# Kernel tuning notes

Hardware: AMD Instinct MI355X
Metric: run time of the kernel (lower is better)

The kernel has to match this reference:

```python
import jax, jax.numpy as jnp
import numpy as np

B, S, D, H, M = 4, 512, 768, 12, 4
DFF = 4 * D
HD = D // H
EPS = 1e-6  # timm/jvp_layers LayerNorm eps
SCALE = HD ** -0.5


def _ln(x, g, b):
    mu = jnp.mean(x, axis=-1, keepdims=True)
    var = jnp.mean((x - mu) ** 2, axis=-1, keepdims=True)
    return (x - mu) * jax.lax.rsqrt(var + EPS) * g + b


def _block(x, g1, b1, Wqkv, Wproj, bproj, g2, b2, W1, bf1, W2, bf2):
    # pre-norm attention
    h = _ln(x, g1, b1)
    qkv = h @ Wqkv                       # [B,S,3D]
    q, k, v = jnp.split(qkv, 3, axis=-1)
    q = q.reshape(B, S, H, HD)
    k = k.reshape(B, S, H, HD)
    v = v.reshape(B, S, H, HD)
    scores = jnp.einsum('bqhd,bkhd->bhqk', q, k) * SCALE
    attn = jax.nn.softmax(scores, axis=-1)
    o = jnp.einsum('bhqk,bkhd->bqhd', attn, v).reshape(B, S, D)
    x = x + o @ Wproj + bproj
    # pre-norm MLP
    h2 = _ln(x, g2, b2)
    mlp = jax.nn.gelu(h2 @ W1 + bf1, approximate=False) @ W2 + bf2
    return x + mlp


def setup_inputs() -> dict:
    key = jax.random.key(0)
    ks = jax.random.split(key, 8)
    w = 0.02
    return {
        'x': jax.random.normal(ks[0], (B, S, D), jnp.float32),
        'x_tangent': jax.random.normal(ks[1], (B, M, S, D), jnp.float32),
        'g1': jnp.ones((D,), jnp.float32),
        'b1': jnp.zeros((D,), jnp.float32),
        'Wqkv': jax.random.normal(ks[2], (D, 3 * D), jnp.float32) * w,
        'Wproj': jax.random.normal(ks[3], (D, D), jnp.float32) * w,
        'bproj': jnp.zeros((D,), jnp.float32),
        'g2': jnp.ones((D,), jnp.float32),
        'b2': jnp.zeros((D,), jnp.float32),
        'W1': jax.random.normal(ks[4], (D, DFF), jnp.float32) * w,
        'bf1': jnp.zeros((DFF,), jnp.float32),
        'W2': jax.random.normal(ks[5], (DFF, D), jnp.float32) * w,
        'bf2': jnp.zeros((D,), jnp.float32),
    }


def reference(x, x_tangent, g1, b1, Wqkv, Wproj, bproj, g2, b2, W1, bf1, W2, bf2):
    f = lambda xx: _block(xx, g1, b1, Wqkv, Wproj, bproj, g2, b2, W1, bf1, W2, bf2)
    # linearize once: primal + efficient JVP for all M tangent directions
    out, jvp_fn = jax.linearize(f, x)
    out_tangent = jax.vmap(jvp_fn, in_axes=1, out_axes=1)(x_tangent)  # [B,M,S,D]
    return out, out_tangent
```

## Files before the change

kernel.cpp:

```cpp
#include <hip/hip_runtime.h>
#include <math.h>

constexpr int B_ = 4, S_ = 512, D_ = 768, H_ = 12, M_ = 4, DFF_ = 3072, HD_ = 64;
constexpr float EPS_ = 1e-6f;
constexpr float SCALE_ = 0.125f;
constexpr int BS_ = B_ * S_;
constexpr int BH_ = B_ * H_;
constexpr long long BSD_ = (long long)BS_ * D_;
constexpr long long BS3D_ = (long long)BS_ * 3 * D_;
constexpr long long ATT_ = (long long)BH_ * S_ * S_;
constexpr long long BSF_ = (long long)BS_ * DFF_;

typedef __attribute__((ext_vector_type(8))) short bf16x8;
typedef __attribute__((ext_vector_type(4))) float f32x4;

__device__ __forceinline__ ushort f2bf(float f) {
    uint32_t u = __float_as_uint(f);
    u += 0x7FFF + ((u >> 16) & 1);
    return (ushort)(u >> 16);
}
__device__ __forceinline__ float bf2f(ushort u) {
    return __uint_as_float((uint32_t)u << 16);
}

__device__ __forceinline__ void gll16(const ushort* g, ushort* l) {
    __builtin_amdgcn_global_load_lds((const __attribute__((address_space(1))) void*)g,
                                     (__attribute__((address_space(3))) void*)l, 16, 0, 0);
}

template <int N> __device__ __forceinline__ void waitcnt_vm() {
    if constexpr (N == 0) asm volatile("s_waitcnt vmcnt(0)" ::: "memory");
    else if constexpr (N == 4) asm volatile("s_waitcnt vmcnt(4)" ::: "memory");
    else if constexpr (N == 6) asm volatile("s_waitcnt vmcnt(6)" ::: "memory");
    else if constexpr (N == 8) asm volatile("s_waitcnt vmcnt(8)" ::: "memory");
    else static_assert(N == 0 || N == 4 || N == 6 || N == 8, "add literal");
}

__device__ __forceinline__ void waitcnt_lgkm0() {
    asm volatile("s_waitcnt lgkmcnt(0)" ::: "memory");
    __builtin_amdgcn_sched_barrier(0);
}

__device__ __forceinline__ int xcd_swz(int flat, int nwg) {
    int q = nwg >> 3, r = nwg & 7;
    int x = flat & 7, pos = flat >> 3;
    int base = (x < r) ? x * (q + 1) : r * (q + 1) + (x - r) * q;
    return base + pos;
}

__device__ __forceinline__ size_t stroff(int rg, int c, int Nc) {
    int m = rg >> 11;
    int b = (rg >> 9) & (B_ - 1);
    int s = rg & (S_ - 1);
    return ((size_t)((b * M_ + m) * S_ + s)) * Nc + c;
}

__device__ __forceinline__ float block_sum(float v) {
    __shared__ float red[4];
    int tid = threadIdx.x;
#pragma unroll
    for (int off = 32; off > 0; off >>= 1) v += __shfl_down(v, off, 64);
    __syncthreads();
    if ((tid & 63) == 0) red[tid >> 6] = v;
    __syncthreads();
    return red[0] + red[1] + red[2] + red[3];
}

__device__ __forceinline__ float block_max(float v) {
    __shared__ float red[4];
    int tid = threadIdx.x;
#pragma unroll
    for (int off = 32; off > 0; off >>= 1) v = fmaxf(v, __shfl_down(v, off, 64));
    __syncthreads();
    if ((tid & 63) == 0) red[tid >> 6] = v;
    __syncthreads();
    return fmaxf(fmaxf(red[0], red[1]), fmaxf(red[2], red[3]));
}

__global__ __launch_bounds__(256) void transpose_f2b(const float* __restrict__ W,
                                                     ushort* __restrict__ WT,
                                                     int K, int N) {
    __shared__ float t[32][33];
    int n0 = blockIdx.x * 32, k0 = blockIdx.y * 32;
    int tx = threadIdx.x & 31, ty = threadIdx.x >> 5;
#pragma unroll
    for (int i = 0; i < 4; i++)
        t[ty + i * 8][tx] = W[(size_t)(k0 + ty + i * 8) * N + n0 + tx];
    __syncthreads();
#pragma unroll
    for (int i = 0; i < 4; i++)
        WT[(size_t)(n0 + ty + i * 8) * K + k0 + tx] = f2bf(t[tx][ty + i * 8]);
}

__global__ __launch_bounds__(256) void transpose_v(const ushort* __restrict__ src0,
                                                   ushort* __restrict__ Vt0,
                                                   ushort* __restrict__ dVt4) {
    int z = blockIdx.z;
    int m = z / BH_, bh = z % BH_;
    const ushort* qkvb = src0 + (size_t)m * BS3D_;
    ushort* Vt = (m == 0) ? Vt0 : dVt4 + (size_t)(m - 1) * BSD_;
    int b = bh / H_, hh = bh - b * H_;
    int s0 = blockIdx.x * 32, d0 = blockIdx.y * 32;
    __shared__ ushort t[32][33];
    int tx = threadIdx.x & 31, ty = threadIdx.x >> 5;
#pragma unroll
    for (int i = 0; i < 4; i++)
        t[ty + i * 8][tx] = qkvb[(size_t)(b * S_ + s0 + ty + i * 8) * 3 * D_ + 2 * D_ + hh * HD_ + d0 + tx];
    __syncthreads();
#pragma unroll
    for (int i = 0; i < 4; i++)
        Vt[(size_t)bh * HD_ * S_ + (size_t)(d0 + ty + i * 8) * S_ + s0 + tx] = t[tx][ty + i * 8];
}

__global__ __launch_bounds__(256) void ln_fwd(const float* __restrict__ x,
                                              const float* __restrict__ g,
                                              const float* __restrict__ bta,
                                              ushort* __restrict__ xhat,
                                              ushort* __restrict__ h,
                                              float* __restrict__ rstd) {
    int row = blockIdx.x;
    const float* xr = x + (size_t)row * D_;
    int tid = threadIdx.x;
    float v[3];
    float s = 0.f;
#pragma unroll
    for (int i = 0; i < 3; i++) { v[i] = xr[tid + i * 256]; s += v[i]; }
    s = block_sum(s);
    float mu = s * (1.0f / D_);
    float vs = 0.f;
#pragma unroll
    for (int i = 0; i < 3; i++) { float c = v[i] - mu; vs += c * c; }
    vs = block_sum(vs);
    float rs = rsqrtf(vs * (1.0f / D_) + EPS_);
#pragma unroll
    for (int i = 0; i < 3; i++) {
        int c = tid + i * 256;
        float xh = (v[i] - mu) * rs;
        xhat[(size_t)row * D_ + c] = f2bf(xh);
        h[(size_t)row * D_ + c] = f2bf(xh * g[c] + bta[c]);
    }
    if (tid == 0) rstd[row] = rs;
}

__global__ __launch_bounds__(256) void ln_jvp(const float* __restrict__ tf,
                                              const ushort* __restrict__ tb, int mode,
                                              const ushort* __restrict__ xhat,
                                              const float* __restrict__ rstd,
                                              const float* __restrict__ g,
                                              ushort* __restrict__ dh,
                                              ushort* __restrict__ xtb) {
    int rg = blockIdx.x;
    int r = rg & (BS_ - 1);
    size_t pbase = (size_t)r * D_;
    int tid = threadIdx.x;
    float tv[3], xh[3];
    float s1 = 0.f, s2 = 0.f;
    size_t tbase;
    if (mode == 0) {
        int m = rg >> 11;
        int b = r >> 9, s = r & (S_ - 1);
        tbase = ((size_t)((b * M_ + m) * S_ + s)) * D_;
    } else {
        tbase = (size_t)rg * D_;
    }
#pragma unroll
    for (int i = 0; i < 3; i++) {
        int c = tid + i * 256;
        tv[i] = (mode == 0) ? tf[tbase + c] : bf2f(tb[tbase + c]);
        xh[i] = bf2f(xhat[pbase + c]);
        s1 += tv[i];
        s2 += tv[i] * xh[i];
    }
    s1 = block_sum(s1);
    s2 = block_sum(s2);
    float mt = s1 * (1.0f / D_);
    float mx = s2 * (1.0f / D_);
    float rs = rstd[r];
#pragma unroll
    for (int i = 0; i < 3; i++) {
        int c = tid + i * 256;
        dh[(size_t)rg * D_ + c] = f2bf(g[c] * rs * (tv[i] - mt - xh[i] * mx));
        if (mode == 0 && xtb) xtb[(size_t)rg * D_ + c] = f2bf(tv[i]);
    }
}

template <int BM, int BN, int EPI, bool RS, bool OS>
__global__ __launch_bounds__(256) void gemm_mfma(const ushort* __restrict__ A,
                                                 const ushort* __restrict__ BT,
                                                 const float* __restrict__ bias,
                                                 const float* __restrict__ resf,
                                                 const ushort* __restrict__ resb,
                                                 float* __restrict__ Cf,
                                                 ushort* __restrict__ Cb,
                                                 ushort* __restrict__ aux,
                                                 int Nc, int Kd) {
    constexpr int FI = BM / 32, FJ = BN / 32;
    constexpr int LA = BM / 32, LB = BN / 32, L = LA + LB;
    __shared__ ushort As[2][BM * 64];
    __shared__ ushort Bs[2][BN * 64];
    int tid = threadIdx.x;
    int wave = tid >> 6, lane = tid & 63;
    int wr = wave >> 1, wc = wave & 1;
    int gx = gridDim.x, nwg = gx * gridDim.y;
    int work = xcd_swz(blockIdx.x + blockIdx.y * gx, nwg);
    int band = work / (8 * gx);
    int wi = work - band * (8 * gx);
    int row0 = (band * 8 + (wi & 7)) * BM;
    int col0 = (wi >> 3) * BN;

    int srow = lane >> 3;
    int skel = ((lane & 7) ^ (lane >> 3)) * 8;
    const ushort* Ag0 = A + (size_t)(row0 + srow) * Kd + skel;
    const ushort* Bg0 = BT + (size_t)(col0 + srow) * Kd + skel;

    auto stage = [&](int bufi, int k0) {
#pragma unroll
        for (int cc = 0; cc < LA; cc++) {
            int c = wave * LA + cc;
            gll16(Ag0 + (size_t)(c * 8) * Kd + k0, As[bufi] + c * 512);
        }
#pragma unroll
        for (int cc = 0; cc < LB; cc++) {
            int c = wave * LB + cc;
            gll16(Bg0 + (size_t)(c * 8) * Kd + k0, Bs[bufi] + c * 512);
        }
    };

    int frow = lane & 15, fkb = (lane >> 4) * 8;
    int aoff[2][FI], boff[2][FJ];
#pragma unroll
    for (int ks = 0; ks < 2; ks++) {
        int sw = (fkb + ks * 32) ^ ((frow & 7) * 8);
#pragma unroll
        for (int i = 0; i < FI; i++) aoff[ks][i] = (wr * (BM / 2) + i * 16 + frow) * 64 + sw;
#pragma unroll
        for (int j = 0; j < FJ; j++) boff[ks][j] = (wc * (BN / 2) + j * 16 + frow) * 64 + sw;
    }

    f32x4 acc[FI][FJ] = {};

    int nt = Kd >> 6;
    stage(0, 0);
    if (nt > 1) { stage(1, 64); waitcnt_vm<L>(); }
    else        { waitcnt_vm<0>(); }
    __builtin_amdgcn_s_barrier();
    __builtin_amdgcn_sched_barrier(0);

    int cur = 0;
    for (int t = 0; t < nt; t++) {
        bf16x8 af[2][FI], bfv[2][FJ];
        const ushort* Ab = As[cur];
        const ushort* Bb = Bs[cur];
#pragma unroll
        for (int ks = 0; ks < 2; ks++) {
#pragma unroll
            for (int i = 0; i < FI; i++) af[ks][i] = *(const bf16x8*)(Ab + aoff[ks][i]);
#pragma unroll
            for (int j = 0; j < FJ; j++) bfv[ks][j] = *(const bf16x8*)(Bb + boff[ks][j]);
        }
        waitcnt_lgkm0();
        __builtin_amdgcn_s_barrier();
        if (t + 2 < nt) {
            stage(cur, (t + 2) << 6);
            __builtin_amdgcn_sched_barrier(0);
        }
#pragma unroll
        for (int ks = 0; ks < 2; ks++)
#pragma unroll
            for (int i = 0; i < FI; i++)
#pragma unroll
                for (int j = 0; j < FJ; j++)
                    acc[i][j] = __builtin_amdgcn_mfma_f32_16x16x32_bf16(af[ks][i], bfv[ks][j], acc[i][j], 0, 0, 0);
        __builtin_amdgcn_sched_barrier(0);
        if (t + 2 < nt) waitcnt_vm<L>();
        else if (t + 1 < nt) waitcnt_vm<0>();
        __builtin_amdgcn_s_barrier();
        __builtin_amdgcn_sched_barrier(0);
        cur ^= 1;
    }

#pragma unroll
    for (int i = 0; i < FI; i++) {
        int rbase = row0 + wr * (BM / 2) + i * 16 + (lane >> 4) * 4;
#pragma unroll
        for (int j = 0; j < FJ; j++) {
            int c = col0 + wc * (BN / 2) + j * 16 + (lane & 15);
#pragma unroll
            for (int r = 0; r < 4; r++) {
                int rg = rbase + r;
                size_t off = (size_t)rg * Nc + c;
                float v = acc[i][j][r];
                if (EPI == 0) {
                    if (bias) v += bias[c];
                    if (resf) v += resf[RS ? stroff(rg, c, Nc) : off];
                    if (resb) v += bf2f(resb[off]);
                    if (Cf) { if (OS) Cf[stroff(rg, c, Nc)] = v; else Cf[off] = v; }
                    if (Cb) Cb[off] = f2bf(v);
                } else if (EPI == 1) {
                    v += bias[c];
                    float cdf = 0.5f * (1.0f + erff(v * 0.70710678118654752f));
                    Cb[off] = f2bf(v * cdf);
                    aux[off] = f2bf(cdf + v * 0.39894228040143267f * expf(-0.5f * v * v));
                } else {
                    Cb[off] = f2bf(v * bf2f(aux[(size_t)(rg & (BS_ - 1)) * Nc + c]));
                }
            }
        }
    }
}

template <bool TAN>
__global__ __launch_bounds__(256) void attn_qk_mfma(const ushort* __restrict__ qkvb,
                                                    const ushort* __restrict__ dqkvp,
                                                    ushort* __restrict__ sc) {
    int work = xcd_swz(blockIdx.x, gridDim.x);
    constexpr int NT = S_ / 128;
    int mz = work / (BH_ * NT * NT);
    int rem = work % (BH_ * NT * NT);
    int bh = rem / (NT * NT);
    int r2 = rem % (NT * NT);
    int q0 = (r2 / NT) * 128, kc0 = (r2 % NT) * 128;
    int b = bh / H_, hh = bh - b * H_;
    const size_t qoff = (size_t)b * S_ * 3 * D_ + hh * HD_;
    const int ld = 3 * D_;
    const ushort* dqkv = TAN ? dqkvp + (size_t)mz * BS3D_ : nullptr;
    __shared__ ushort As[128 * 64];
    __shared__ ushort Bs[128 * 64];
    __shared__ ushort dAs[TAN ? 128 * 64 : 1];
    __shared__ ushort dBs[TAN ? 128 * 64 : 1];
    int tid = threadIdx.x;
    int wave = tid >> 6, lane = tid & 63;
    int wr = wave >> 1, wc = wave & 1;

    int srow = lane >> 3;
    int skel = ((lane & 7) ^ (lane >> 3)) * 8;
    const ushort* Ag0 = qkvb + qoff + (size_t)(q0 + srow) * ld + skel;
    const ushort* Bg0 = qkvb + qoff + D_ + (size_t)(kc0 + srow) * ld + skel;

#pragma unroll
    for (int cc = 0; cc < 4; cc++) {
        int c = wave * 4 + cc;
        gll16(Ag0 + (size_t)(c * 8) * ld, As + c * 512);
        gll16(Bg0 + (size_t)(c * 8) * ld, Bs + c * 512);
        if (TAN) {
            gll16(dqkv + qoff + (size_t)(q0 + c * 8 + srow) * ld + skel, dAs + c * 512);
            gll16(dqkv + qoff + D_ + (size_t)(kc0 + c * 8 + srow) * ld + skel, dBs + c * 512);
        }
    }
    __syncthreads();

    int frow = lane & 15, fkb = (lane >> 4) * 8;
    f32x4 acc[4][4] = {};
#pragma unroll
    for (int ks = 0; ks < 2; ks++) {
        int sw = (fkb + ks * 32) ^ ((frow & 7) * 8);
        bf16x8 af[4], bfv[4];
#pragma unroll
        for (int i = 0; i < 4; i++) af[i] = *(const bf16x8*)(As + (wr * 64 + i * 16 + frow) * 64 + sw);
#pragma unroll
        for (int j = 0; j < 4; j++) bfv[j] = *(const bf16x8*)(Bs + (wc * 64 + j * 16 + frow) * 64 + sw);
        if (!TAN) {
#pragma unroll
            for (int i = 0; i < 4; i++)
#pragma unroll
                for (int j = 0; j < 4; j++)
                    acc[i][j] = __builtin_amdgcn_mfma_f32_16x16x32_bf16(af[i], bfv[j], acc[i][j], 0, 0, 0);
        } else {
            bf16x8 daf[4], dbf[4];
#pragma unroll
            for (int i = 0; i < 4; i++) daf[i] = *(const bf16x8*)(dAs + (wr * 64 + i * 16 + frow) * 64 + sw);
#pragma unroll
            for (int j = 0; j < 4; j++) dbf[j] = *(const bf16x8*)(dBs + (wc * 64 + j * 16 + frow) * 64 + sw);
#pragma unroll
            for (int i = 0; i < 4; i++)
#pragma unroll
                for (int j = 0; j < 4; j++) {
                    acc[i][j] = __builtin_amdgcn_mfma_f32_16x16x32_bf16(daf[i], bfv[j], acc[i][j], 0, 0, 0);
                    acc[i][j] = __builtin_amdgcn_mfma_f32_16x16x32_bf16(af[i], dbf[j], acc[i][j], 0, 0, 0);
                }
        }
    }

    ushort* scm = sc + (size_t)mz * ATT_;
#pragma unroll
    for (int i = 0; i < 4; i++) {
        int rbase = q0 + wr * 64 + i * 16 + (lane >> 4) * 4;
#pragma unroll
        for (int j = 0; j < 4; j++) {
            int c = kc0 + wc * 64 + j * 16 + (lane & 15);
#pragma unroll
            for (int r = 0; r < 4; r++)
                scm[((size_t)bh * S_ + rbase + r) * S_ + c] = f2bf(acc[i][j][r] * SCALE_);
        }
    }
}

__global__ __launch_bounds__(256) void attn_av_p(const ushort* __restrict__ Pb,
                                                 const ushort* __restrict__ Vt,
                                                 ushort* __restrict__ outp) {
    int work = xcd_swz(blockIdx.x, gridDim.x);
    constexpr int NT = S_ / 128;
    int bh = work / NT;
    int q0 = (work % NT) * 128;
    int b = bh / H_, hh = bh - b * H_;
    const ushort* Pg = Pb + (size_t)bh * S_ * S_;
    const ushort* Vg = Vt + (size_t)bh * HD_ * S_;
    __shared__ ushort As[128 * 64];
    __shared__ ushort Bs[64 * 64];
    int tid = threadIdx.x;
    int wave = tid >> 6, lane = tid & 63;
    int wr = wave >> 1, wc = wave & 1;
    int srow = lane >> 3;
    int skel = ((lane & 7) ^ (lane >> 3)) * 8;
    int frow = lane & 15, fkb = (lane >> 4) * 8;

    f32x4 acc[4][2] = {};
    for (int k0 = 0; k0 < S_; k0 += 64) {
#pragma unroll
        for (int cc = 0; cc < 4; cc++) {
            int c = wave * 4 + cc;
            gll16(Pg + (size_t)(q0 + c * 8 + srow) * S_ + k0 + skel, As + c * 512);
        }
#pragma unroll
        for (int cc = 0; cc < 2; cc++) {
            int c = wave * 2 + cc;
            gll16(Vg + (size_t)(c * 8 + srow) * S_ + k0 + skel, Bs + c * 512);
        }
        __syncthreads();
#pragma unroll
        for (int ks = 0; ks < 2; ks++) {
            int sw = (fkb + ks * 32) ^ ((frow & 7) * 8);
            bf16x8 af[4], bfv[2];
#pragma unroll
            for (int i = 0; i < 4; i++) af[i] = *(const bf16x8*)(As + (wr * 64 + i * 16 + frow) * 64 + sw);
#pragma unroll
            for (int j = 0; j < 2; j++) bfv[j] = *(const bf16x8*)(Bs + (wc * 32 + j * 16 + frow) * 64 + sw);
#pragma unroll
            for (int i = 0; i < 4; i++)
#pragma unroll
                for (int j = 0; j < 2; j++)
                    acc[i][j] = __builtin_amdgcn_mfma_f32_16x16x32_bf16(af[i], bfv[j], acc[i][j], 0, 0, 0);
        }
        __syncthreads();
    }

#pragma unroll
    for (int i = 0; i < 4; i++) {
        int rbase = q0 + wr * 64 + i * 16 + (lane >> 4) * 4;
#pragma unroll
        for (int j = 0; j < 2; j++) {
            int c = hh * HD_ + wc * 32 + j * 16 + (lane & 15);
#pragma unroll
            for (int r = 0; r < 4; r++)
                outp[(size_t)(b * S_ + rbase + r) * D_ + c] = f2bf(acc[i][j][r]);
        }
    }
}

__global__ __launch_bounds__(256) void attn_av_tan(const ushort* __restrict__ Pb,
                                                   const ushort* __restrict__ dscp,
                                                   const ushort* __restrict__ Vt,
                                                   const ushort* __restrict__ dVtp,
                                                   const ushort* __restrict__ Ob,
                                                   ushort* __restrict__ outp) {
    int work = xcd_swz(blockIdx.x, gridDim.x);
    int mz = work / (BH_ * 4);
    int rem = work % (BH_ * 4);
    int bh = rem / 4;
    int q0 = (rem % 4) * 128;
    int b = bh / H_, hh = bh - b * H_;
    const ushort* Pg = Pb + (size_t)bh * S_ * S_;
    const ushort* Dg = dscp + (size_t)mz * ATT_ + (size_t)bh * S_ * S_;
    const ushort* Vg = Vt + (size_t)bh * HD_ * S_;
    const ushort* dVg = dVtp + (size_t)mz * BSD_ + (size_t)bh * HD_ * S_;
    ushort* outm = outp + (size_t)mz * BSD_;
    __shared__ ushort Ps[128 * 64], Ds[128 * 64], Vs[64 * 64], dVs[64 * 64];
    int tid = threadIdx.x;
    int wave = tid >> 6, lane = tid & 63;
    int wr = wave >> 1, wc = wave & 1;
    int srow = lane >> 3;
    int skel = ((lane & 7) ^ (lane >> 3)) * 8;
    int frow = lane & 15, fkb = (lane >> 4) * 8;
    int aoff[2][4], boff[2][2];
#pragma unroll
    for (int ks = 0; ks < 2; ks++) {
        int sw = (fkb + ks * 32) ^ ((frow & 7) * 8);
#pragma unroll
        for (int i = 0; i < 4; i++) aoff[ks][i] = (wr * 64 + i * 16 + frow) * 64 + sw;
#pragma unroll
        for (int j = 0; j < 2; j++) boff[ks][j] = (wc * 32 + j * 16 + frow) * 64 + sw;
    }

    float s[4] = {0.f, 0.f, 0.f, 0.f};
    f32x4 acc[4][2] = {};

    for (int k0 = 0; k0 < S_; k0 += 64) {
#pragma unroll
        for (int cc = 0; cc < 4; cc++) {
            int c = wave * 4 + cc;
            gll16(Pg + (size_t)(q0 + c * 8 + srow) * S_ + k0 + skel, Ps + c * 512);
            gll16(Dg + (size_t)(q0 + c * 8 + srow) * S_ + k0 + skel, Ds + c * 512);
        }
#pragma unroll
        for (int cc = 0; cc < 2; cc++) {
            int c = wave * 2 + cc;
            gll16(Vg + (size_t)(c * 8 + srow) * S_ + k0 + skel, Vs + c * 512);
            gll16(dVg + (size_t)(c * 8 + srow) * S_ + k0 + skel, dVs + c * 512);
        }
        __syncthreads();
#pragma unroll
        for (int ks = 0; ks < 2; ks++) {
            bf16x8 p8[4], pq8[4], v8[2], dv8[2];
#pragma unroll
            for (int i = 0; i < 4; i++) {
                p8[i] = *(const bf16x8*)(Ps + aoff[ks][i]);
                bf16x8 d8 = *(const bf16x8*)(Ds + aoff[ks][i]);
#pragma unroll
                for (int e = 0; e < 8; e++) {
                    float pd = bf2f((ushort)p8[i][e]) * bf2f((ushort)d8[e]);
                    s[i] += pd;
                    pq8[i][e] = (short)f2bf(pd);
                }
            }
#pragma unroll
            for (int j = 0; j < 2; j++) {
                v8[j] = *(const bf16x8*)(Vs + boff[ks][j]);
                dv8[j] = *(const bf16x8*)(dVs + boff[ks][j]);
            }
#pragma unroll
            for (int i = 0; i < 4; i++)
#pragma unroll
                for (int j = 0; j < 2; j++) {
                    acc[i][j] = __builtin_amdgcn_mfma_f32_16x16x32_bf16(pq8[i], v8[j], acc[i][j], 0, 0, 0);
                    acc[i][j] = __builtin_amdgcn_mfma_f32_16x16x32_bf16(p8[i], dv8[j], acc[i][j], 0, 0, 0);
                }
        }
        __syncthreads();
    }

#pragma unroll
    for (int i = 0; i < 4; i++) {
        s[i] += __shfl_xor(s[i], 16);
        s[i] += __shfl_xor(s[i], 32);
    }

#pragma unroll
    for (int i = 0; i < 4; i++) {
        int rbase = q0 + wr * 64 + i * 16 + (lane >> 4) * 4;
#pragma unroll
        for (int r = 0; r < 4; r++) {
            float sc = __shfl(s[i], ((lane >> 4) << 2) + r);
#pragma unroll
            for (int j = 0; j < 2; j++) {
                int c = hh * HD_ + wc * 32 + j * 16 + (lane & 15);
                float o = bf2f(Ob[(size_t)(b * S_ + rbase + r) * D_ + c]);
                outm[(size_t)(b * S_ + rbase + r) * D_ + c] = f2bf(acc[i][j][r] - sc * o);
            }
        }
    }
}

__global__ __launch_bounds__(256) void softmax_rows(const ushort* __restrict__ sc,
                                                    ushort* __restrict__ scb) {
    size_t row = blockIdx.x;
    const ushort* p = sc + row * S_;
    int tid = threadIdx.x;
    ushort2 vu = *(const ushort2*)&p[tid * 2];
    float v0 = bf2f(vu.x), v1 = bf2f(vu.y);
    float mx = block_max(fmaxf(v0, v1));
    float e0 = expf(v0 - mx), e1 = expf(v1 - mx);
    float s = block_sum(e0 + e1);
    float inv = 1.0f / s;
    ushort2 ob; ob.x = f2bf(e0 * inv); ob.y = f2bf(e1 * inv);
    *(ushort2*)&scb[row * S_ + tid * 2] = ob;
}

extern "C" void kernel_launch(void* const* d_in, const int* in_sizes, int n_in,
                              void* d_out, int out_size, void* d_ws, size_t ws_size,
                              hipStream_t stream) {
    const float* x = (const float*)d_in[0];
    const float* xt = (const float*)d_in[1];
    const float* g1 = (const float*)d_in[2];
    const float* b1 = (const float*)d_in[3];
    const float* Wqkv = (const float*)d_in[4];
    const float* Wproj = (const float*)d_in[5];
    const float* bproj = (const float*)d_in[6];
    const float* g2 = (const float*)d_in[7];
    const float* b2 = (const float*)d_in[8];
    const float* W1 = (const float*)d_in[9];
    const float* bf1 = (const float*)d_in[10];
    const float* W2 = (const float*)d_in[11];
    const float* bf2 = (const float*)d_in[12];
    float* out = (float*)d_out;
    float* out_t = out + BSD_;

    char* wp = (char*)d_ws;
    auto alloc = [&](size_t bytes) { void* p = wp; wp += (bytes + 255) & ~(size_t)255; return p; };
    ushort* xhat1 = (ushort*)alloc(BSD_ * 2);
    ushort* hb5 = (ushort*)alloc(5 * BSD_ * 2);
    ushort* obb = (ushort*)alloc(BSD_ * 2);
    float* x2 = (float*)alloc(BSD_ * 4);
    ushort* xhat2 = (ushort*)alloc(BSD_ * 2);
    ushort* h2b = (ushort*)alloc(BSD_ * 2);
    ushort* dx2b = (ushort*)alloc(4 * BSD_ * 2);
    ushort* xt_b = (ushort*)alloc(4 * BSD_ * 2);
    ushort* Vt = (ushort*)alloc(BSD_ * 2);
    ushort* dscb2 = (ushort*)alloc(2 * ATT_ * 2);
    ushort* attnb = (ushort*)alloc(ATT_ * 2);
    ushort* gpb = (ushort*)alloc(BSF_ * 2);
    float* rstd1 = (float*)alloc(BS_ * 4);
    float* rstd2 = (float*)alloc(BS_ * 4);
    ushort* WqkvT = (ushort*)alloc((size_t)D_ * 3 * D_ * 2);
    ushort* WprojT = (ushort*)alloc((size_t)D_ * D_ * 2);
    ushort* W1T = (ushort*)alloc((size_t)DFF_ * D_ * 2);
    ushort* W2T = (ushort*)alloc((size_t)D_ * DFF_ * 2);
    char* regA = (char*)alloc(4 * BSF_ * 2);
    ushort* qkv5 = (ushort*)regA;
    ushort* da4 = (ushort*)regA;
    ushort* dVt4 = (ushort*)alloc(4 * BSD_ * 2);
    char* regB = (char*)alloc(4 * BSD_ * 2);
    ushort* ab = (ushort*)regB;
    ushort* dob4 = (ushort*)regB;
    ushort* dh2_4 = (ushort*)regB;

    transpose_f2b<<<dim3(3 * D_ / 32, D_ / 32), 256, 0, stream>>>(Wqkv, WqkvT, D_, 3 * D_);
    transpose_f2b<<<dim3(D_ / 32, D_ / 32), 256, 0, stream>>>(Wproj, WprojT, D_, D_);
    transpose_f2b<<<dim3(DFF_ / 32, D_ / 32), 256, 0, stream>>>(W1, W1T, D_, DFF_);
    transpose_f2b<<<dim3(D_ / 32, DFF_ / 32), 256, 0, stream>>>(W2, W2T, DFF_, D_);

    ln_fwd<<<BS_, 256, 0, stream>>>(x, g1, b1, xhat1, hb5, rstd1);
    ln_jvp<<<4 * BS_, 256, 0, stream>>>(xt, nullptr, 0, xhat1, rstd1, g1, hb5 + BSD_, xt_b);
    gemm_mfma<128, 128, 0, false, false><<<dim3(3 * D_ / 128, 5 * BS_ / 128), 256, 0, stream>>>(
        hb5, WqkvT, nullptr, nullptr, nullptr, nullptr, qkv5, nullptr, 3 * D_, D_);
    transpose_v<<<dim3(S_ / 32, HD_ / 32, 5 * BH_), 256, 0, stream>>>(qkv5, Vt, dVt4);

    attn_qk_mfma<false><<<(S_ / 128) * (S_ / 128) * BH_, 256, 0, stream>>>(qkv5, nullptr, dscb2);
    softmax_rows<<<BH_ * S_, 256, 0, stream>>>(dscb2, attnb);
    attn_av_p<<<(S_ / 128) * BH_, 256, 0, stream>>>(attnb, Vt, obb);
    gemm_mfma<64, 64, 0, false, false><<<dim3(D_ / 64, BS_ / 64), 256, 0, stream>>>(
        obb, WprojT, bproj, x, nullptr, x2, nullptr, nullptr, D_, D_);
    ln_fwd<<<BS_, 256, 0, stream>>>(x2, g2, b2, xhat2, h2b, rstd2);
    gemm_mfma<128, 128, 1, false, false><<<dim3(DFF_ / 128, BS_ / 128), 256, 0, stream>>>(
        h2b, W1T, bf1, nullptr, nullptr, nullptr, ab, gpb, DFF_, D_);
    gemm_mfma<64, 64, 0, false, false><<<dim3(D_ / 64, BS_ / 64), 256, 0, stream>>>(
        ab, W2T, bf2, x2, nullptr, out, nullptr, nullptr, D_, DFF_);

    const ushort* dqkv4 = qkv5 + BS3D_;
    for (int p = 0; p < 2; p++) {
        attn_qk_mfma<true><<<2 * (S_ / 128) * (S_ / 128) * BH_, 256, 0, stream>>>(
            qkv5, dqkv4 + (size_t)p * 2 * BS3D_, dscb2);
        attn_av_tan<<<2 * 4 * BH_, 256, 0, stream>>>(
            attnb, dscb2, Vt, dVt4 + (size_t)p * 2 * BSD_, obb, dob4 + (size_t)p * 2 * BSD_);
    }
    gemm_mfma<128, 64, 0, false, false><<<dim3(D_ / 64, 4 * BS_ / 128), 256, 0, stream>>>(
        dob4, WprojT, nullptr, nullptr, xt_b, nullptr, dx2b, nullptr, D_, D_);
    ln_jvp<<<4 * BS_, 256, 0, stream>>>(nullptr, dx2b, 1, xhat2, rstd2, g2, dh2_4, nullptr);
    gemm_mfma<128, 128, 2, false, false><<<dim3(DFF_ / 128, 4 * BS_ / 128), 256, 0, stream>>>(
        dh2_4, W1T, nullptr, nullptr, nullptr, nullptr, da4, gpb, DFF_, D_);
    gemm_mfma<128, 64, 0, false, true><<<dim3(D_ / 64, 4 * BS_ / 128), 256, 0, stream>>>(
        da4, W2T, nullptr, nullptr, dx2b, out_t, nullptr, nullptr, D_, DFF_);
}
```

Baseline: 443.8 us.

## Batch primal and tangent projection/MLP-down GEMMs into single stacked launches

Stacks the primal attention output with the four tangent outputs, and the primal GELU activations with the tangent MLP activations, into contiguous buffers. The Wproj GEMM and the W2 GEMM then each run once over 5*BS rows instead of as separate primal and tangent launches. Row-dependent epilogues (EPI 4/5) apply the bias and residual for primal rows and the tangent residual for the others. The primal residual stream x2 is now kept in bf16 and LayerNorm reads it from bf16, which lowers precision of the residual. This cuts launches and small under-occupied 64x64 GEMMs at the cost of a branchy epilogue and a reworked buffer aliasing plan.

```diff
diff --git a/kernel.cpp b/kernel.cpp
--- a/kernel.cpp
+++ b/kernel.cpp
@@ -112,19 +112,24 @@
         Vt[(size_t)bh * HD_ * S_ + (size_t)(d0 + ty + i * 8) * S_ + s0 + tx] = t[tx][ty + i * 8];
 }
 
-__global__ __launch_bounds__(256) void ln_fwd(const float* __restrict__ x,
+__global__ __launch_bounds__(256) void ln_fwd(const float* __restrict__ xf,
+                                              const ushort* __restrict__ xb,
                                               const float* __restrict__ g,
                                               const float* __restrict__ bta,
                                               ushort* __restrict__ xhat,
                                               ushort* __restrict__ h,
                                               float* __restrict__ rstd) {
     int row = blockIdx.x;
-    const float* xr = x + (size_t)row * D_;
+    size_t base = (size_t)row * D_;
     int tid = threadIdx.x;
     float v[3];
     float s = 0.f;
 #pragma unroll
-    for (int i = 0; i < 3; i++) { v[i] = xr[tid + i * 256]; s += v[i]; }
+    for (int i = 0; i < 3; i++) {
+        int c = tid + i * 256;
+        v[i] = xf ? xf[base + c] : bf2f(xb[base + c]);
+        s += v[i];
+    }
     s = block_sum(s);
     float mu = s * (1.0f / D_);
     float vs = 0.f;
@@ -136,8 +141,8 @@
     for (int i = 0; i < 3; i++) {
         int c = tid + i * 256;
         float xh = (v[i] - mu) * rs;
-        xhat[(size_t)row * D_ + c] = f2bf(xh);
-        h[(size_t)row * D_ + c] = f2bf(xh * g[c] + bta[c]);
+        xhat[base + c] = f2bf(xh);
+        h[base + c] = f2bf(xh * g[c] + bta[c]);
     }
     if (tid == 0) rstd[row] = rs;
 }
@@ -184,13 +189,15 @@
     }
 }
 
-template <int BM, int BN, int EPI, bool RS, bool OS>
+template <int BM, int BN, int EPI>
 __global__ __launch_bounds__(256) void gemm_mfma(const ushort* __restrict__ A,
                                                  const ushort* __restrict__ BT,
                                                  const float* __restrict__ bias,
                                                  const float* __restrict__ resf,
                                                  const ushort* __restrict__ resb,
+                                                 const ushort* __restrict__ resb2,
                                                  float* __restrict__ Cf,
+                                                 float* __restrict__ Cf2,
                                                  ushort* __restrict__ Cb,
                                                  ushort* __restrict__ aux,
                                                  int Nc, int Kd) {
@@ -291,18 +298,32 @@
                 size_t off = (size_t)rg * Nc + c;
                 float v = acc[i][j][r];
                 if (EPI == 0) {
-                    if (bias) v += bias[c];
-                    if (resf) v += resf[RS ? stroff(rg, c, Nc) : off];
-                    if (resb) v += bf2f(resb[off]);
-                    if (Cf) { if (OS) Cf[stroff(rg, c, Nc)] = v; else Cf[off] = v; }
-                    if (Cb) Cb[off] = f2bf(v);
+                    Cb[off] = f2bf(v);
                 } else if (EPI == 1) {
                     v += bias[c];
                     float cdf = 0.5f * (1.0f + erff(v * 0.70710678118654752f));
                     Cb[off] = f2bf(v * cdf);
                     aux[off] = f2bf(cdf + v * 0.39894228040143267f * expf(-0.5f * v * v));
+                } else if (EPI == 2) {
+                    Cb[off] = f2bf(v * bf2f(aux[(size_t)(rg & (BS_ - 1)) * Nc + c]));
+                } else if (EPI == 4) {
+                    if (rg < BS_) {
+                        v += bias[c] + bf2f(resb[off]);
+                        Cf[off] = v;
+                    } else {
+                        int rg2 = rg - BS_;
+                        v += bf2f(resb2[(size_t)rg2 * Nc + c]);
+                        Cf2[stroff(rg2, c, Nc)] = v;
+                    }
                 } else {
-                    Cb[off] = f2bf(v * bf2f(aux[(size_t)(rg & (BS_ - 1)) * Nc + c]));
+                    if (rg < BS_) {
+                        v += bias[c] + resf[off];
+                        Cb[off] = f2bf(v);
+                    } else {
+                        int rg2 = rg - BS_;
+                        v += bf2f(resb[(size_t)rg2 * Nc + c]);
+                        aux[(size_t)rg2 * Nc + c] = f2bf(v);
+                    }
                 }
             }
         }
@@ -596,10 +617,13 @@
 
     char* wp = (char*)d_ws;
     auto alloc = [&](size_t bytes) { void* p = wp; wp += (bytes + 255) & ~(size_t)255; return p; };
+    char* regBig = (char*)alloc(25 * BSD_ * 2);
+    ushort* hb5 = (ushort*)regBig;
+    ushort* ob5 = (ushort*)(regBig + 5 * BSD_ * 2);
+    ushort* qkv5 = (ushort*)(regBig + 10 * BSD_ * 2);
+    ushort* ab5 = (ushort*)regBig;
     ushort* xhat1 = (ushort*)alloc(BSD_ * 2);
-    ushort* hb5 = (ushort*)alloc(5 * BSD_ * 2);
-    ushort* obb = (ushort*)alloc(BSD_ * 2);
-    float* x2 = (float*)alloc(BSD_ * 4);
+    ushort* x2b = xhat1;
     ushort* xhat2 = (ushort*)alloc(BSD_ * 2);
     ushort* h2b = (ushort*)alloc(BSD_ * 2);
     ushort* dx2b = (ushort*)alloc(4 * BSD_ * 2);
@@ -608,55 +632,47 @@
     ushort* dscb2 = (ushort*)alloc(2 * ATT_ * 2);
     ushort* attnb = (ushort*)alloc(ATT_ * 2);
     ushort* gpb = (ushort*)alloc(BSF_ * 2);
+    ushort* dh2_4 = (ushort*)alloc(4 * BSD_ * 2);
+    ushort* dVt4 = (ushort*)alloc(4 * BSD_ * 2);
     float* rstd1 = (float*)alloc(BS_ * 4);
     float* rstd2 = (float*)alloc(BS_ * 4);
     ushort* WqkvT = (ushort*)alloc((size_t)D_ * 3 * D_ * 2);
     ushort* WprojT = (ushort*)alloc((size_t)D_ * D_ * 2);
     ushort* W1T = (ushort*)alloc((size_t)DFF_ * D_ * 2);
     ushort* W2T = (ushort*)alloc((size_t)D_ * DFF_ * 2);
-    char* regA = (char*)alloc(4 * BSF_ * 2);
-    ushort* qkv5 = (ushort*)regA;
-    ushort* da4 = (ushort*)regA;
-    ushort* dVt4 = (ushort*)alloc(4 * BSD_ * 2);
-    char* regB = (char*)alloc(4 * BSD_ * 2);
-    ushort* ab = (ushort*)regB;
-    ushort* dob4 = (ushort*)regB;
-    ushort* dh2_4 = (ushort*)regB;
 
     transpose_f2b<<<dim3(3 * D_ / 32, D_ / 32), 256, 0, stream>>>(Wqkv, WqkvT, D_, 3 * D_);
     transpose_f2b<<<dim3(D_ / 32, D_ / 32), 256, 0, stream>>>(Wproj, WprojT, D_, D_);
     transpose_f2b<<<dim3(DFF_ / 32, D_ / 32), 256, 0, stream>>>(W1, W1T, D_, DFF_);
     transpose_f2b<<<dim3(D_ / 32, DFF_ / 32), 256, 0, stream>>>(W2, W2T, DFF_, D_);
 
-    ln_fwd<<<BS_, 256, 0, stream>>>(x, g1, b1, xhat1, hb5, rstd1);
+    ln_fwd<<<BS_, 256, 0, stream>>>(x, nullptr, g1, b1, xhat1, hb5, rstd1);
     ln_jvp<<<4 * BS_, 256, 0, stream>>>(xt, nullptr, 0, xhat1, rstd1, g1, hb5 + BSD_, xt_b);
-    gemm_mfma<128, 128, 0, false, false><<<dim3(3 * D_ / 128, 5 * BS_ / 128), 256, 0, stream>>>(
-        hb5, WqkvT, nullptr, nullptr, nullptr, nullptr, qkv5, nullptr, 3 * D_, D_);
+    gemm_mfma<128, 128, 0><<<dim3(3 * D_ / 128, 5 * BS_ / 128), 256, 0, stream>>>(
+        hb5, WqkvT, nullptr, nullptr, nullptr, nullptr, nullptr, nullptr, qkv5, nullptr, 3 * D_, D_);
     transpose_v<<<dim3(S_ / 32, HD_ / 32, 5 * BH_), 256, 0, stream>>>(qkv5, Vt, dVt4);
 
     attn_qk_mfma<false><<<(S_ / 128) * (S_ / 128) * BH_, 256, 0, stream>>>(qkv5, nullptr, dscb2);
     softmax_rows<<<BH_ * S_, 256, 0, stream>>>(dscb2, attnb);
-    attn_av_p<<<(S_ / 128) * BH_, 256, 0, stream>>>(attnb, Vt, obb);
-    gemm_mfma<64, 64, 0, false, false><<<dim3(D_ / 64, BS_ / 64), 256, 0, stream>>>(
-        obb, WprojT, bproj, x, nullptr, x2, nullptr, nullptr, D_, D_);
-    ln_fwd<<<BS_, 256, 0, stream>>>(x2, g2, b2, xhat2, h2b, rstd2);
-    gemm_mfma<128, 128, 1, false, false><<<dim3(DFF_ / 128, BS_ / 128), 256, 0, stream>>>(
-        h2b, W1T, bf1, nullptr, nullptr, nullptr, ab, gpb, DFF_, D_);
-    gemm_mfma<64, 64, 0, false, false><<<dim3(D_ / 64, BS_ / 64), 256, 0, stream>>>(
-        ab, W2T, bf2, x2, nullptr, out, nullptr, nullptr, D_, DFF_);
+    attn_av_p<<<(S_ / 128) * BH_, 256, 0, stream>>>(attnb, Vt, ob5);
 
     const ushort* dqkv4 = qkv5 + BS3D_;
     for (int p = 0; p < 2; p++) {
         attn_qk_mfma<true><<<2 * (S_ / 128) * (S_ / 128) * BH_, 256, 0, stream>>>(
             qkv5, dqkv4 + (size_t)p * 2 * BS3D_, dscb2);
         attn_av_tan<<<2 * 4 * BH_, 256, 0, stream>>>(
-            attnb, dscb2, Vt, dVt4 + (size_t)p * 2 * BSD_, obb, dob4 + (size_t)p * 2 * BSD_);
-    }
-    gemm_mfma<128, 64, 0, false, false><<<dim3(D_ / 64, 4 * BS_ / 128), 256, 0, stream>>>(
-        dob4, WprojT, nullptr, nullptr, xt_b, nullptr, dx2b, nullptr, D_, D_);
+            attnb, dscb2, Vt, dVt4 + (size_t)p * 2 * BSD_, ob5, ob5 + BSD_ + (size_t)p * 2 * BSD_);
+    }
+
+    gemm_mfma<128, 64, 5><<<dim3(D_ / 64, 5 * BS_ / 128), 256, 0, stream>>>(
+        ob5, WprojT, bproj, x, xt_b, nullptr, nullptr, nullptr, x2b, dx2b, D_, D_);
+
+    ln_fwd<<<BS_, 256, 0, stream>>>(nullptr, x2b, g2, b2, xhat2, h2b, rstd2);
+    gemm_mfma<128, 128, 1><<<dim3(DFF_ / 128, BS_ / 128), 256, 0, stream>>>(
+        h2b, W1T, bf1, nullptr, nullptr, nullptr, nullptr, nullptr, ab5, gpb, DFF_, D_);
     ln_jvp<<<4 * BS_, 256, 0, stream>>>(nullptr, dx2b, 1, xhat2, rstd2, g2, dh2_4, nullptr);
-    gemm_mfma<128, 128, 2, false, false><<<dim3(DFF_ / 128, 4 * BS_ / 128), 256, 0, stream>>>(
-        dh2_4, W1T, nullptr, nullptr, nullptr, nullptr, da4, gpb, DFF_, D_);
-    gemm_mfma<128, 64, 0, false, true><<<dim3(D_ / 64, 4 * BS_ / 128), 256, 0, stream>>>(
-        da4, W2T, nullptr, nullptr, dx2b, out_t, nullptr, nullptr, D_, DFF_);
-}
+    gemm_mfma<128, 128, 2><<<dim3(DFF_ / 128, 4 * BS_ / 128), 256, 0, stream>>>(
+        dh2_4, W1T, nullptr, nullptr, nullptr, nullptr, nullptr, nullptr, ab5 + BSF_, gpb, DFF_, D_);
+    gemm_mfma<128, 64, 4><<<dim3(D_ / 64, 5 * BS_ / 128), 256, 0, stream>>>(
+        ab5, W2T, bf2, nullptr, x2b, dx2b, out, out_t, nullptr, nullptr, D_, DFF_);
+}
```

New measurement: 435.5 us. Within noise of the previous version (-1.9%).
